# Kernel tuning notes

Measured on AMD Instinct MI355X. Metric: run time of the kernel, lower is better.

The kernel has to match this reference:

```python
import jax, jax.numpy as jnp
import numpy as np

V, E, H, S, B, MAX_OOV = 50000, 256, 512, 500, 64, 50


def setup_inputs() -> dict:
    key = jax.random.key(0)
    ks = jax.random.split(key, 22)
    s = 0.02  # param init scale
    return {
        "input_token": jax.random.randint(ks[0], (B, 1), 0, V),
        "encoder_hidden_states": jax.random.normal(ks[1], (S, B, 2 * H), jnp.float32),
        "projected_encoder_hidden_states": jax.random.normal(ks[2], (S, B, H), jnp.float32),
        "src_mask": jnp.ones((B, S), dtype=bool),
        "prev_hidden": jax.random.normal(ks[3], (1, B, H), jnp.float32),
        "encoder_batch_extended_vocab": jax.random.randint(ks[4], (B, S), 0, V + MAX_OOV),
        "batch_max_oov": MAX_OOV,
        # learned parameters
        "emb": jax.random.normal(ks[5], (V, E), jnp.float32) * s,
        "attn_Wq": jax.random.normal(ks[6], (H, H), jnp.float32) * s,   # query_layer, no bias
        "attn_We": jax.random.normal(ks[7], (1, H), jnp.float32) * s,   # energy_layer, no bias
        "gru_Wih": jax.random.normal(ks[8], (3 * H, E + 2 * H), jnp.float32) * s,
        "gru_Whh": jax.random.normal(ks[9], (3 * H, H), jnp.float32) * s,
        "gru_bih": jax.random.normal(ks[10], (3 * H,), jnp.float32) * s,
        "gru_bhh": jax.random.normal(ks[11], (3 * H,), jnp.float32) * s,
        "lin_W": jax.random.normal(ks[12], (H, E + 3 * H), jnp.float32) * s,
        "lin_b": jax.random.normal(ks[13], (H,), jnp.float32) * s,
        "pg_W": jax.random.normal(ks[14], (1, E + 3 * H), jnp.float32) * s,
        "pg_b": jax.random.normal(ks[15], (1,), jnp.float32) * s,
        "out_W": jax.random.normal(ks[16], (V, H), jnp.float32) * s,
        "out_b": jax.random.normal(ks[17], (V,), jnp.float32) * s,
    }


def _forward(input_token, enc_h, proj_key, prev_hidden, ext_vocab, max_oov,
             emb, attn_Wq, attn_We, gru_Wih, gru_Whh, gru_bih, gru_bhh,
             lin_W, lin_b, pg_W, pg_b, out_W, out_b):
    b = input_token.shape[0]
    embed = jnp.transpose(emb[input_token], (1, 0, 2))  # [1,B,E]

    # Bahdanau attention (softmax over source dim 0; mask unused, as in source)
    q = jnp.einsum('tbh,oh->tbo', prev_hidden, attn_Wq)            # [1,B,H]
    scores = jnp.einsum('sbh,oh->sb', jnp.tanh(q + proj_key), attn_We)  # [S,B]
    alphas = jax.nn.softmax(scores, axis=0)                        # [S,B]
    context = jnp.einsum('sb,sbd->bd', alphas, enc_h)[None]        # [1,B,2H]
    attention_dist = alphas.T                                      # [B,S]

    # GRU cell (torch gate order: r, z, n)
    x = jnp.concatenate([embed, context], axis=2)[0]               # [B,E+2H]
    h = prev_hidden[0]                                             # [B,H]
    gi = x @ gru_Wih.T + gru_bih                                   # [B,3H]
    gh = h @ gru_Whh.T + gru_bhh
    i_r, i_z, i_n = jnp.split(gi, 3, axis=1)
    h_r, h_z, h_n = jnp.split(gh, 3, axis=1)
    r = jax.nn.sigmoid(i_r + h_r)
    z = jax.nn.sigmoid(i_z + h_z)
    n = jnp.tanh(i_n + r * h_n)
    h_new = (1.0 - z) * n + z * h                                  # [B,H]
    rnn_output = h_new[None]                                       # [1,B,H]

    concat = jnp.concatenate([embed, rnn_output, context], axis=2)  # [1,B,E+3H]
    p_gen = jax.nn.sigmoid(jnp.einsum('tbf,of->tbo', concat, pg_W) + pg_b)  # [1,B,1]
    lin = jnp.einsum('tbf,of->tbo', concat, lin_W) + lin_b          # [1,B,H]
    logits = jnp.einsum('tbh,vh->tbv', lin, out_W) + out_b          # [1,B,V]

    gen_prob = p_gen * jax.nn.softmax(logits, axis=2)               # [1,B,V]
    attn_prob = ((1.0 - p_gen) * attention_dist[None])[0]           # [B,S]

    ext = jnp.concatenate(
        [gen_prob, jnp.zeros((1, b, max_oov), gen_prob.dtype)], axis=2) + 1e-12  # [1,B,V+oov]
    rows = jnp.arange(b)[:, None]
    merged = ext.at[0, rows, ext_vocab].add(attn_prob)              # scatter_add over vocab dim
    output = jnp.log(merged)
    return output, h_new[None]


def reference(input_token, encoder_hidden_states, projected_encoder_hidden_states,
              src_mask, prev_hidden, encoder_batch_extended_vocab, batch_max_oov,
              emb, attn_Wq, attn_We, gru_Wih, gru_Whh, gru_bih, gru_bhh,
              lin_W, lin_b, pg_W, pg_b, out_W, out_b):
    return _forward(input_token, encoder_hidden_states, projected_encoder_hidden_states,
                    prev_hidden, encoder_batch_extended_vocab, batch_max_oov,
                    emb, attn_Wq, attn_We, gru_Wih, gru_Whh, gru_bih, gru_bhh,
                    lin_W, lin_b, pg_W, pg_b, out_W, out_b)
```

## Files before the change

kernel.cpp:

```cpp
#include <hip/hip_runtime.h>
#include <hip/hip_bf16.h>
#include <math.h>

namespace {
constexpr int V = 50000, E = 256, H = 512, S = 500, B = 64, OOVN = 50;
constexpr int VEXT = V + OOVN;
constexpr int CCAT = E + 3 * H;
constexpr int G3 = 3 * H;

typedef __attribute__((ext_vector_type(8))) short short8;
typedef __attribute__((ext_vector_type(4))) float f32x4;

__device__ __forceinline__ float wsum(float v) {
#pragma unroll
  for (int off = 32; off > 0; off >>= 1) v += __shfl_xor(v, off, 64);
  return v;
}
__device__ __forceinline__ float sigmoidf(float x) { return 1.f / (1.f + __expf(-x)); }
__device__ __forceinline__ float fast_tanh(float x) {
  x = fminf(fmaxf(x, -15.f), 15.f);
  float e = __expf(2.f * x);
  return __fdividef(e - 1.f, e + 1.f);
}
__device__ __forceinline__ void smerge(float& m, float& l, float om, float ol) {
  float nm = fmaxf(m, om);
  l = l * __expf(m - nm) + ol * __expf(om - nm);
  m = nm;
}

__device__ __forceinline__ short bf16_rn_s(float f) {
  __hip_bfloat16 h = __float2bfloat16(f);
  return __builtin_bit_cast(short, h);
}
__device__ __forceinline__ void hilo1(float f, short* hi, short* lo) {
  unsigned u = __float_as_uint(f);
  *hi = (short)(u >> 16);
  *lo = bf16_rn_s(f - __uint_as_float(u & 0xffff0000u));
}
__device__ __forceinline__ void hilo8(float4 a, float4 b, short8& hi, short8& lo) {
  float f[8] = {a.x, a.y, a.z, a.w, b.x, b.y, b.z, b.w};
#pragma unroll
  for (int i = 0; i < 8; ++i) {
    unsigned u = __float_as_uint(f[i]);
    hi[i] = (short)(u >> 16);
    lo[i] = bf16_rn_s(f[i] - __uint_as_float(u & 0xffff0000u));
  }
}

template <int KSTEPS>
__device__ __forceinline__ void gemm16(const short* __restrict__ Xhi,
                                       const short* __restrict__ Xlo, int ldx, int xk0,
                                       const float* __restrict__ W, int ldw, int wk0,
                                       int n0, const float* __restrict__ bias,
                                       float* __restrict__ C, int ldc) {
  const int l = threadIdx.x & 63;
  const int r16 = l & 15, q16 = l >> 4;
  f32x4 acc[4];
#pragma unroll
  for (int t = 0; t < 4; ++t) acc[t] = (f32x4){0.f, 0.f, 0.f, 0.f};

  const float* wp = W + (size_t)(n0 + r16) * ldw + wk0 + q16 * 8;
  const short* xh[4];
  const short* xl[4];
#pragma unroll
  for (int t = 0; t < 4; ++t) {
    int row = t * 16 + r16;
    xh[t] = Xhi + (size_t)row * ldx + xk0 + q16 * 8;
    xl[t] = Xlo + (size_t)row * ldx + xk0 + q16 * 8;
  }

#pragma unroll
  for (int ks = 0; ks < KSTEPS; ++ks) {
    const int ko = ks * 32;
    float4 w0 = *reinterpret_cast<const float4*>(wp + ko);
    float4 w1 = *reinterpret_cast<const float4*>(wp + ko + 4);
    short8 whi, wlo;
    hilo8(w0, w1, whi, wlo);
#pragma unroll
    for (int t = 0; t < 4; ++t) {
      short8 ah = *reinterpret_cast<const short8*>(xh[t] + ko);
      short8 al = *reinterpret_cast<const short8*>(xl[t] + ko);
      acc[t] = __builtin_amdgcn_mfma_f32_16x16x32_bf16(ah, whi, acc[t], 0, 0, 0);
      acc[t] = __builtin_amdgcn_mfma_f32_16x16x32_bf16(al, whi, acc[t], 0, 0, 0);
      acc[t] = __builtin_amdgcn_mfma_f32_16x16x32_bf16(ah, wlo, acc[t], 0, 0, 0);
    }
  }
  float bv = bias ? bias[n0 + r16] : 0.f;
#pragma unroll
  for (int t = 0; t < 4; ++t) {
#pragma unroll
    for (int r = 0; r < 4; ++r) {
      int row = t * 16 + q16 * 4 + r;
      C[(size_t)row * ldc + n0 + r16] = acc[t][r] + bv;
    }
  }
}

__global__ void k_prep(const int* __restrict__ tok, const float* __restrict__ emb,
                       const float* __restrict__ prevh, float* __restrict__ cc,
                       short* __restrict__ cch, short* __restrict__ ccl,
                       short* __restrict__ hh, short* __restrict__ hl) {
  int i = blockIdx.x * 256 + threadIdx.x;
  hilo1(prevh[i], &hh[i], &hl[i]);
  if (i < 16384) {
    int b = i >> 8, e = i & 255;
    float v = emb[(size_t)tok[b] * E + e];
    cc[b * CCAT + e] = v;
    hilo1(v, &cch[b * CCAT + e], &ccl[b * CCAT + e]);
  }
}

__global__ void __launch_bounds__(256) k_gemm_q(const short* __restrict__ hh,
                                                const short* __restrict__ hl,
                                                const float* __restrict__ Wq,
                                                float* __restrict__ qpart) {
  int w = blockIdx.x * 4 + (threadIdx.x >> 6);
  int c = w >> 5, nt = w & 31;
  gemm16<8>(hh, hl, H, c * 256, Wq, H, c * 256, nt * 16, nullptr,
            qpart + (size_t)c * 64 * H, H);
}

__global__ void k_scores(const float* __restrict__ qpart, const float* __restrict__ pk,
                         const float* __restrict__ We, float* __restrict__ scores) {
  int lane = threadIdx.x & 63;
  int gw = blockIdx.x * 4 + (threadIdx.x >> 6);
  int s = gw >> 6, b = gw & 63;
  const float* q0 = qpart + b * H + lane * 8;
  const float* q1 = q0 + 64 * H;
  const float* kr = pk + ((size_t)s * B + b) * H + lane * 8;
  const float* er = We + lane * 8;
  float part = 0.f;
#pragma unroll
  for (int i = 0; i < 2; ++i) {
    float4 qa = *reinterpret_cast<const float4*>(q0 + i * 4);
    float4 qb = *reinterpret_cast<const float4*>(q1 + i * 4);
    float4 kv = *reinterpret_cast<const float4*>(kr + i * 4);
    float4 ev = *reinterpret_cast<const float4*>(er + i * 4);
    part += fast_tanh(qa.x + qb.x + kv.x) * ev.x + fast_tanh(qa.y + qb.y + kv.y) * ev.y +
            fast_tanh(qa.z + qb.z + kv.z) * ev.z + fast_tanh(qa.w + qb.w + kv.w) * ev.w;
  }
  part = wsum(part);
  if (lane == 0) scores[s * B + b] = part;
}

__global__ void k_softmax_s(const float* __restrict__ scores, float* __restrict__ alphasT) {
  int b = blockIdx.x, t = threadIdx.x;
  int w = t >> 6, lane = t & 63;
  __shared__ float rm[8], rl[8];
  float v = (t < S) ? scores[t * B + b] : -INFINITY;
  float m = v;
#pragma unroll
  for (int off = 32; off > 0; off >>= 1) m = fmaxf(m, __shfl_xor(m, off, 64));
  if (lane == 0) rm[w] = m;
  __syncthreads();
  float bm = rm[0];
#pragma unroll
  for (int i = 1; i < 8; ++i) bm = fmaxf(bm, rm[i]);
  float e = (t < S) ? __expf(v - bm) : 0.f;
  float sw = wsum(e);
  if (lane == 0) rl[w] = sw;
  __syncthreads();
  float tot = rl[0];
#pragma unroll
  for (int i = 1; i < 8; ++i) tot += rl[i];
  if (t < S) alphasT[b * S + t] = e / tot;
}

__global__ void k_ctx(const float* __restrict__ alphasT, const float* __restrict__ ench,
                      float* __restrict__ ctxp) {
  int b = blockIdx.x, chf = blockIdx.y, sh = blockIdx.z;
  int t = threadIdx.x;
  __shared__ float sa[250];
  if (t < 250) sa[t] = alphasT[b * S + sh * 250 + t];
  __syncthreads();
  const float* base = ench + ((size_t)(sh * 250) * B + b) * 1024 + chf * 512 + t;
  float a0 = 0.f, a1 = 0.f;
#pragma unroll 8
  for (int s = 0; s < 250; s += 2) {
    a0 += sa[s] * base[(size_t)s * (B * 1024)];
    a1 += sa[s + 1] * base[(size_t)(s + 1) * (B * 1024)];
  }
  ctxp[((sh * B + b) * 1024) + chf * 512 + t] = a0 + a1;
}

__global__ void k_ctx2(const float* __restrict__ ctxp, float* __restrict__ cc,
                       short* __restrict__ cch, short* __restrict__ ccl) {
  int b = blockIdx.x, t = threadIdx.x;
  int c = t * 4;
  float4 v0 = *reinterpret_cast<const float4*>(&ctxp[(b * 1024) + c]);
  float4 v1 = *reinterpret_cast<const float4*>(&ctxp[((B + b) * 1024) + c]);
  float r[4] = {v0.x + v1.x, v0.y + v1.y, v0.z + v1.z, v0.w + v1.w};
#pragma unroll
  for (int i = 0; i < 4; ++i) {
    int col = 768 + c + i;
    cc[b * CCAT + col] = r[i];
    hilo1(r[i], &cch[b * CCAT + col], &ccl[b * CCAT + col]);
  }
}

__global__ void __launch_bounds__(256) k_gemm_gru(
    const short* __restrict__ cch, const short* __restrict__ ccl,
    const short* __restrict__ hh, const short* __restrict__ hl,
    const float* __restrict__ Wih, const float* __restrict__ Whh,
    float* __restrict__ gip, float* __restrict__ ghp) {
  int w = blockIdx.x * 4 + (threadIdx.x >> 6);
  if (w < 480) {
    int c = w / 96, nt = w % 96;
    int xk0 = (c == 0) ? 0 : 768 + (c - 1) * 256;
    int wk0 = c * 256;
    gemm16<8>(cch, ccl, CCAT, xk0, Wih, 1280, wk0, nt * 16, nullptr,
              gip + (size_t)c * 64 * G3, G3);
  } else {
    int w2 = w - 480;
    int c = w2 / 96, nt = w2 % 96;
    gemm16<8>(hh, hl, H, c * 256, Whh, H, c * 256, nt * 16, nullptr,
              ghp + (size_t)c * 64 * G3, G3);
  }
}

__global__ void k_gates(const float* __restrict__ gip, const float* __restrict__ ghp,
                        const float* __restrict__ bih, const float* __restrict__ bhh,
                        const float* __restrict__ prevh, const float* __restrict__ pgW,
                        const float* __restrict__ pgb, float* __restrict__ cc,
                        short* __restrict__ cch, short* __restrict__ ccl,
                        float* __restrict__ hout, float* __restrict__ pgsum) {
  int b = blockIdx.x, j = threadIdx.x;
  float ir = bih[j], iz = bih[512 + j], in_ = bih[1024 + j];
#pragma unroll
  for (int c = 0; c < 5; ++c) {
    const float* g = gip + (size_t)c * 64 * G3 + b * G3;
    ir += g[j]; iz += g[512 + j]; in_ += g[1024 + j];
  }
  float hr = bhh[j], hz = bhh[512 + j], hn = bhh[1024 + j];
#pragma unroll
  for (int c = 0; c < 2; ++c) {
    const float* g = ghp + (size_t)c * 64 * G3 + b * G3;
    hr += g[j]; hz += g[512 + j]; hn += g[1024 + j];
  }
  float r = sigmoidf(ir + hr);
  float z = sigmoidf(iz + hz);
  float n = fast_tanh(in_ + r * hn);
  float h = prevh[b * H + j];
  float hnew = (1.f - z) * n + z * h;
  hout[b * H + j] = hnew;
  cc[b * CCAT + E + j] = hnew;
  hilo1(hnew, &cch[b * CCAT + E + j], &ccl[b * CCAT + E + j]);
  float acc = hnew * pgW[E + j];
  acc += cc[b * CCAT + 768 + j] * pgW[768 + j];
  acc += cc[b * CCAT + 1280 + j] * pgW[1280 + j];
  if (j < 256) acc += cc[b * CCAT + j] * pgW[j];
  acc = wsum(acc);
  __shared__ float sl[8];
  int w = j >> 6, lane = j & 63;
  if (lane == 0) sl[w] = acc;
  __syncthreads();
  if (j == 0) {
    float tot = pgb[0];
#pragma unroll
    for (int i = 0; i < 8; ++i) tot += sl[i];
    pgsum[b] = tot;
  }
}

__global__ void __launch_bounds__(256) k_gemm_lin(const short* __restrict__ cch,
                                                  const short* __restrict__ ccl,
                                                  const float* __restrict__ linW,
                                                  float* __restrict__ linpart) {
  int w = blockIdx.x * 4 + (threadIdx.x >> 6);
  int c = w >> 5, nt = w & 31;
  gemm16<8>(cch, ccl, CCAT, c * 256, linW, CCAT, c * 256, nt * 16, nullptr,
            linpart + (size_t)c * 64 * H, H);
}

__global__ void k_linfin(const float* __restrict__ linpart, const float* __restrict__ linb,
                         short* __restrict__ lh) {
  int idx = blockIdx.x * 256 + threadIdx.x;
  int b = idx >> 9, o = idx & 511;
  float v = linb[o];
#pragma unroll
  for (int c = 0; c < 7; ++c) v += linpart[(size_t)c * 64 * H + b * H + o];
  lh[idx] = bf16_rn_s(v);
}

__global__ void __launch_bounds__(512, 4) k_gemm_logits(
    const short* __restrict__ lh, const float* __restrict__ outW,
    const float* __restrict__ outb, float* __restrict__ logits) {
  __shared__ __align__(16) short xs[64 * 512];
  char* xb = reinterpret_cast<char*>(xs);
  int tid = threadIdx.x;
#pragma unroll
  for (int k = 0; k < 8; ++k) {
    int m = k * 512 + tid;
    int row = m >> 6;
    short8 v = *reinterpret_cast<const short8*>(lh + (size_t)m * 8);
    int byte = (m * 16) ^ ((row & 7) << 4);
    *reinterpret_cast<short8*>(xb + byte) = v;
  }
  __syncthreads();
  const int l = tid & 63;
  const int r16 = l & 15, q16 = l >> 4;
  const int waveId = blockIdx.x * 8 + (tid >> 6);
  if (waveId >= V / 16) return;
  const int n0 = waveId * 16;
  f32x4 acc[4];
#pragma unroll
  for (int t = 0; t < 4; ++t) acc[t] = (f32x4){0.f, 0.f, 0.f, 0.f};
  const float* wp = outW + (size_t)(n0 + r16) * H + q16 * 8;
  int arow[4], aswz[4];
#pragma unroll
  for (int t = 0; t < 4; ++t) {
    int row = t * 16 + r16;
    arow[t] = row * 1024 + q16 * 16;
    aswz[t] = (row & 7) << 4;
  }
#pragma unroll
  for (int ks = 0; ks < 16; ++ks) {
    float4 w0 = *reinterpret_cast<const float4*>(wp + ks * 32);
    float4 w1 = *reinterpret_cast<const float4*>(wp + ks * 32 + 4);
    short8 wh;
    wh[0] = bf16_rn_s(w0.x); wh[1] = bf16_rn_s(w0.y);
    wh[2] = bf16_rn_s(w0.z); wh[3] = bf16_rn_s(w0.w);
    wh[4] = bf16_rn_s(w1.x); wh[5] = bf16_rn_s(w1.y);
    wh[6] = bf16_rn_s(w1.z); wh[7] = bf16_rn_s(w1.w);
#pragma unroll
    for (int t = 0; t < 4; ++t) {
      short8 a = *reinterpret_cast<const short8*>(xb + ((arow[t] + ks * 64) ^ aswz[t]));
      acc[t] = __builtin_amdgcn_mfma_f32_16x16x32_bf16(a, wh, acc[t], 0, 0, 0);
    }
  }
  float bv = outb[n0 + r16];
#pragma unroll
  for (int t = 0; t < 4; ++t) {
#pragma unroll
    for (int r = 0; r < 4; ++r) {
      int row = t * 16 + q16 * 4 + r;
      logits[(size_t)row * V + n0 + r16] = acc[t][r] + bv;
    }
  }
}

__global__ void k_vmax(const float* __restrict__ logits, float* __restrict__ pm,
                       float* __restrict__ pl) {
  int b = blockIdx.x, c = blockIdx.y, t = threadIdx.x;
  const float* row = logits + (size_t)b * V + c * 5000;
  float m = -INFINITY, l = 0.f;
  for (int i = t; i < 1250; i += 256) {
    float4 v = *reinterpret_cast<const float4*>(&row[i * 4]);
    float mm = fmaxf(fmaxf(v.x, v.y), fmaxf(v.z, v.w));
    float nm = fmaxf(m, mm);
    l = l * __expf(m - nm) + __expf(v.x - nm) + __expf(v.y - nm) + __expf(v.z - nm) +
        __expf(v.w - nm);
    m = nm;
  }
#pragma unroll
  for (int off = 32; off > 0; off >>= 1) {
    float om = __shfl_xor(m, off, 64), ol = __shfl_xor(l, off, 64);
    smerge(m, l, om, ol);
  }
  __shared__ float sm[4], sl[4];
  int w = t >> 6, lane = t & 63;
  if (lane == 0) { sm[w] = m; sl[w] = l; }
  __syncthreads();
  if (t == 0) {
#pragma unroll
    for (int i = 1; i < 4; ++i) smerge(m, l, sm[i], sl[i]);
    pm[b * 10 + c] = m;
    pl[b * 10 + c] = l;
  }
}

__global__ void k_extinit(const float* __restrict__ logits, const float* __restrict__ pm,
                          const float* __restrict__ pl, const float* __restrict__ pgsum,
                          float* __restrict__ out) {
  int b = blockIdx.x, c = blockIdx.y, t = threadIdx.x;
  float m = -INFINITY, l = 0.f;
#pragma unroll
  for (int i = 0; i < 10; ++i) smerge(m, l, pm[b * 10 + i], pl[b * 10 + i]);
  float pg = sigmoidf(pgsum[b]);
  float scale = pg / l;
  const float* lr = logits + (size_t)b * V + c * 5000;
  float* orow = out + (size_t)b * VEXT + c * 5000;
  for (int i = t; i < 2500; i += 256) {
    float2 v = *reinterpret_cast<const float2*>(&lr[i * 2]);
    float2 r;
    r.x = scale * __expf(v.x - m) + 1e-12f;
    r.y = scale * __expf(v.y - m) + 1e-12f;
    *reinterpret_cast<float2*>(&orow[i * 2]) = r;
  }
  if (c == 9 && t < OOVN) out[(size_t)b * VEXT + V + t] = 1e-12f;
}

__constant__ int qbound[5] = {0, 12512, 25024, 37536, 50050};
__global__ void k_scatter_log(const int* __restrict__ extv, const float* __restrict__ alphasT,
                              const float* __restrict__ pgsum, float* __restrict__ out) {
  int b = blockIdx.x >> 2, q = blockIdx.x & 3, t = threadIdx.x;
  int qs0 = qbound[q], qs1 = qbound[q + 1];
  float pg = sigmoidf(pgsum[b]);
  float* row = out + (size_t)b * VEXT;
  for (int s = t; s < S; s += 256) {
    int idx = extv[b * S + s];
    if (idx >= qs0 && idx < qs1) atomicAdd(&row[idx], (1.f - pg) * alphasT[b * S + s]);
  }
  __threadfence();
  __syncthreads();
  int n2 = (qs1 - qs0) >> 1;
  float2* p = reinterpret_cast<float2*>(row + qs0);
  for (int i = t; i < n2; i += 256) {
    float2 v = p[i];
    v.x = logf(v.x);
    v.y = logf(v.y);
    p[i] = v;
  }
  if (((qs1 - qs0) & 1) && t == 0) row[qs1 - 1] = logf(row[qs1 - 1]);
}
}

extern "C" void kernel_launch(void* const* d_in, const int* in_sizes, int n_in,
                              void* d_out, int out_size, void* d_ws, size_t ws_size,
                              hipStream_t stream) {
  const int*   tok   = (const int*)d_in[0];
  const float* ench  = (const float*)d_in[1];
  const float* pk    = (const float*)d_in[2];
  const float* prevh = (const float*)d_in[4];
  const int*   extv  = (const int*)d_in[5];
  const float* emb   = (const float*)d_in[7];
  const float* Wq    = (const float*)d_in[8];
  const float* We    = (const float*)d_in[9];
  const float* Wih   = (const float*)d_in[10];
  const float* Whh   = (const float*)d_in[11];
  const float* bih   = (const float*)d_in[12];
  const float* bhh   = (const float*)d_in[13];
  const float* linW  = (const float*)d_in[14];
  const float* linb  = (const float*)d_in[15];
  const float* pgW   = (const float*)d_in[16];
  const float* pgb   = (const float*)d_in[17];
  const float* outW  = (const float*)d_in[18];
  const float* outb  = (const float*)d_in[19];

  float* out = (float*)d_out;
  float* ws = (float*)d_ws;

  float* qpart   = ws;
  float* scores  = qpart + 65536;
  float* alphasT = scores + 32000;
  float* ctxp    = alphasT + 32000;
  float* cc      = ctxp + 131072;
  float* gip     = cc + 114688;
  float* ghp     = gip + 491520;
  float* linpart = ghp + 196608;
  float* pgsum   = linpart + 229376;
  float* logits  = pgsum + 64;
  float* pm      = logits + 3200000;
  float* pl      = pm + 640;
  short* sp      = (short*)(pl + 640);
  short* cch = sp;
  short* ccl = cch + 114688;
  short* hh  = ccl + 114688;
  short* hl  = hh + 32768;
  short* lh  = hl + 32768;
  float* hout = out + (size_t)B * VEXT;

  k_prep<<<dim3(128), dim3(256), 0, stream>>>(tok, emb, prevh, cc, cch, ccl, hh, hl);
  k_gemm_q<<<dim3(16), dim3(256), 0, stream>>>(hh, hl, Wq, qpart);
  k_scores<<<dim3(8000), dim3(256), 0, stream>>>(qpart, pk, We, scores);
  k_softmax_s<<<dim3(B), dim3(512), 0, stream>>>(scores, alphasT);
  k_ctx<<<dim3(64, 2, 2), dim3(512), 0, stream>>>(alphasT, ench, ctxp);
  k_ctx2<<<dim3(B), dim3(256), 0, stream>>>(ctxp, cc, cch, ccl);
  k_gemm_gru<<<dim3(168), dim3(256), 0, stream>>>(cch, ccl, hh, hl, Wih, Whh, gip, ghp);
  k_gates<<<dim3(B), dim3(512), 0, stream>>>(gip, ghp, bih, bhh, prevh, pgW, pgb, cc, cch,
                                             ccl, hout, pgsum);
  k_gemm_lin<<<dim3(56), dim3(256), 0, stream>>>(cch, ccl, linW, linpart);
  k_linfin<<<dim3(128), dim3(256), 0, stream>>>(linpart, linb, lh);
  k_gemm_logits<<<dim3(391), dim3(512), 0, stream>>>(lh, outW, outb, logits);
  k_vmax<<<dim3(B, 10), dim3(256), 0, stream>>>(logits, pm, pl);
  k_extinit<<<dim3(B, 10), dim3(256), 0, stream>>>(logits, pm, pl, pgsum, out);
  k_scatter_log<<<dim3(256), dim3(256), 0, stream>>>(extv, alphasT, pgsum, out);
}
```

Before: 161.4 us.

## Fuse softmax stats into logits GEMM, merge scatter/log, rebalance GRU/lin GEMMs

The logits GEMM now computes per-block row max and sum-exp partials, which removes the separate vmax pass over the logits. The ext-init, scatter-add and log steps are combined into one kernel that builds each vocab chunk in shared memory, applies the attention scatter there with shared atomics, and writes the log once. This avoids global atomics and the extra read-modify-write passes over the output. The Whh GEMM moves earlier so it runs alongside the query GEMM, now split four ways along K. Most of the lin GEMM moves into the big Wih kernel, leaving only the hidden-state slices after the gates. The trade-off is more launch-time kernels doing mixed work and more partial buffers to reduce.

Result: no change. 162.8 us (+0.8%).

```diff
diff --git a/kernel.cpp b/kernel.cpp
--- a/kernel.cpp
+++ b/kernel.cpp
@@ -7,6 +7,7 @@
 constexpr int VEXT = V + OOVN;
 constexpr int CCAT = E + 3 * H;
 constexpr int G3 = 3 * H;
+constexpr int NLB = 391;
 
 typedef __attribute__((ext_vector_type(8))) short short8;
 typedef __attribute__((ext_vector_type(4))) float f32x4;
@@ -22,8 +23,9 @@
   float e = __expf(2.f * x);
   return __fdividef(e - 1.f, e + 1.f);
 }
-__device__ __forceinline__ void smerge(float& m, float& l, float om, float ol) {
+__device__ __forceinline__ void smerge_s(float& m, float& l, float om, float ol) {
   float nm = fmaxf(m, om);
+  if (nm == -INFINITY) { m = nm; return; }
   l = l * __expf(m - nm) + ol * __expf(om - nm);
   m = nm;
 }
@@ -51,8 +53,7 @@
 __device__ __forceinline__ void gemm16(const short* __restrict__ Xhi,
                                        const short* __restrict__ Xlo, int ldx, int xk0,
                                        const float* __restrict__ W, int ldw, int wk0,
-                                       int n0, const float* __restrict__ bias,
-                                       float* __restrict__ C, int ldc) {
+                                       int n0, float* __restrict__ C, int ldc) {
   const int l = threadIdx.x & 63;
   const int r16 = l & 15, q16 = l >> 4;
   f32x4 acc[4];
@@ -85,13 +86,12 @@
       acc[t] = __builtin_amdgcn_mfma_f32_16x16x32_bf16(ah, wlo, acc[t], 0, 0, 0);
     }
   }
-  float bv = bias ? bias[n0 + r16] : 0.f;
 #pragma unroll
   for (int t = 0; t < 4; ++t) {
 #pragma unroll
     for (int r = 0; r < 4; ++r) {
       int row = t * 16 + q16 * 4 + r;
-      C[(size_t)row * ldc + n0 + r16] = acc[t][r] + bv;
+      C[(size_t)row * ldc + n0 + r16] = acc[t][r];
     }
   }
 }
@@ -110,14 +110,21 @@
   }
 }
 
-__global__ void __launch_bounds__(256) k_gemm_q(const short* __restrict__ hh,
-                                                const short* __restrict__ hl,
-                                                const float* __restrict__ Wq,
-                                                float* __restrict__ qpart) {
+__global__ void __launch_bounds__(256) k_gemm_qgh(
+    const short* __restrict__ hh, const short* __restrict__ hl,
+    const float* __restrict__ Wq, const float* __restrict__ Whh,
+    float* __restrict__ qpart, float* __restrict__ ghp) {
   int w = blockIdx.x * 4 + (threadIdx.x >> 6);
-  int c = w >> 5, nt = w & 31;
-  gemm16<8>(hh, hl, H, c * 256, Wq, H, c * 256, nt * 16, nullptr,
-            qpart + (size_t)c * 64 * H, H);
+  if (w < 128) {
+    int c = w >> 5, nt = w & 31;
+    gemm16<4>(hh, hl, H, c * 128, Wq, H, c * 128, nt * 16,
+              qpart + (size_t)c * 64 * H, H);
+  } else {
+    int w2 = w - 128;
+    int c = w2 / 96, nt = w2 % 96;
+    gemm16<8>(hh, hl, H, c * 256, Whh, H, c * 256, nt * 16,
+              ghp + (size_t)c * 64 * G3, G3);
+  }
 }
 
 __global__ void k_scores(const float* __restrict__ qpart, const float* __restrict__ pk,
@@ -126,18 +133,21 @@
   int gw = blockIdx.x * 4 + (threadIdx.x >> 6);
   int s = gw >> 6, b = gw & 63;
   const float* q0 = qpart + b * H + lane * 8;
-  const float* q1 = q0 + 64 * H;
   const float* kr = pk + ((size_t)s * B + b) * H + lane * 8;
   const float* er = We + lane * 8;
   float part = 0.f;
 #pragma unroll
   for (int i = 0; i < 2; ++i) {
     float4 qa = *reinterpret_cast<const float4*>(q0 + i * 4);
-    float4 qb = *reinterpret_cast<const float4*>(q1 + i * 4);
+    float4 qb = *reinterpret_cast<const float4*>(q0 + 64 * H + i * 4);
+    float4 qc = *reinterpret_cast<const float4*>(q0 + 128 * H + i * 4);
+    float4 qd = *reinterpret_cast<const float4*>(q0 + 192 * H + i * 4);
     float4 kv = *reinterpret_cast<const float4*>(kr + i * 4);
     float4 ev = *reinterpret_cast<const float4*>(er + i * 4);
-    part += fast_tanh(qa.x + qb.x + kv.x) * ev.x + fast_tanh(qa.y + qb.y + kv.y) * ev.y +
-            fast_tanh(qa.z + qb.z + kv.z) * ev.z + fast_tanh(qa.w + qb.w + kv.w) * ev.w;
+    part += fast_tanh(qa.x + qb.x + qc.x + qd.x + kv.x) * ev.x +
+            fast_tanh(qa.y + qb.y + qc.y + qd.y + kv.y) * ev.y +
+            fast_tanh(qa.z + qb.z + qc.z + qd.z + kv.z) * ev.z +
+            fast_tanh(qa.w + qb.w + qc.w + qd.w + kv.w) * ev.w;
   }
   part = wsum(part);
   if (lane == 0) scores[s * B + b] = part;
@@ -198,23 +208,23 @@
   }
 }
 
-__global__ void __launch_bounds__(256) k_gemm_gru(
+__global__ void __launch_bounds__(256) k_gemm_big(
     const short* __restrict__ cch, const short* __restrict__ ccl,
-    const short* __restrict__ hh, const short* __restrict__ hl,
-    const float* __restrict__ Wih, const float* __restrict__ Whh,
-    float* __restrict__ gip, float* __restrict__ ghp) {
+    const float* __restrict__ Wih, const float* __restrict__ linW,
+    float* __restrict__ gip, float* __restrict__ linpart) {
   int w = blockIdx.x * 4 + (threadIdx.x >> 6);
   if (w < 480) {
     int c = w / 96, nt = w % 96;
     int xk0 = (c == 0) ? 0 : 768 + (c - 1) * 256;
     int wk0 = c * 256;
-    gemm16<8>(cch, ccl, CCAT, xk0, Wih, 1280, wk0, nt * 16, nullptr,
+    gemm16<8>(cch, ccl, CCAT, xk0, Wih, 1280, wk0, nt * 16,
               gip + (size_t)c * 64 * G3, G3);
   } else {
     int w2 = w - 480;
-    int c = w2 / 96, nt = w2 % 96;
-    gemm16<8>(hh, hl, H, c * 256, Whh, H, c * 256, nt * 16, nullptr,
-              ghp + (size_t)c * 64 * G3, G3);
+    int c = w2 >> 5, nt = w2 & 31;
+    int k0 = (c == 0) ? 0 : 768 + (c - 1) * 256;
+    gemm16<8>(cch, ccl, CCAT, k0, linW, CCAT, k0, nt * 16,
+              linpart + (size_t)c * 64 * H, H);
   }
 }
 
@@ -262,14 +272,15 @@
   }
 }
 
-__global__ void __launch_bounds__(256) k_gemm_lin(const short* __restrict__ cch,
-                                                  const short* __restrict__ ccl,
-                                                  const float* __restrict__ linW,
-                                                  float* __restrict__ linpart) {
+__global__ void __launch_bounds__(256) k_gemm_linh(const short* __restrict__ cch,
+                                                   const short* __restrict__ ccl,
+                                                   const float* __restrict__ linW,
+                                                   float* __restrict__ linpart) {
   int w = blockIdx.x * 4 + (threadIdx.x >> 6);
   int c = w >> 5, nt = w & 31;
-  gemm16<8>(cch, ccl, CCAT, c * 256, linW, CCAT, c * 256, nt * 16, nullptr,
-            linpart + (size_t)c * 64 * H, H);
+  int k0 = 256 + c * 256;
+  gemm16<8>(cch, ccl, CCAT, k0, linW, CCAT, k0, nt * 16,
+            linpart + (size_t)(5 + c) * 64 * H, H);
 }
 
 __global__ void k_linfin(const float* __restrict__ linpart, const float* __restrict__ linb,
@@ -282,10 +293,12 @@
   lh[idx] = bf16_rn_s(v);
 }
 
-__global__ void __launch_bounds__(512, 4) k_gemm_logits(
+__global__ void __launch_bounds__(512) k_gemm_logits(
     const short* __restrict__ lh, const float* __restrict__ outW,
-    const float* __restrict__ outb, float* __restrict__ logits) {
+    const float* __restrict__ outb, float* __restrict__ logits,
+    float* __restrict__ pm, float* __restrict__ pl) {
   __shared__ __align__(16) short xs[64 * 512];
+  __shared__ float pml[8][64][2];
   char* xb = reinterpret_cast<char*>(xs);
   int tid = threadIdx.x;
 #pragma unroll
@@ -299,119 +312,110 @@
   __syncthreads();
   const int l = tid & 63;
   const int r16 = l & 15, q16 = l >> 4;
-  const int waveId = blockIdx.x * 8 + (tid >> 6);
-  if (waveId >= V / 16) return;
-  const int n0 = waveId * 16;
-  f32x4 acc[4];
-#pragma unroll
-  for (int t = 0; t < 4; ++t) acc[t] = (f32x4){0.f, 0.f, 0.f, 0.f};
-  const float* wp = outW + (size_t)(n0 + r16) * H + q16 * 8;
-  int arow[4], aswz[4];
-#pragma unroll
-  for (int t = 0; t < 4; ++t) {
-    int row = t * 16 + r16;
-    arow[t] = row * 1024 + q16 * 16;
-    aswz[t] = (row & 7) << 4;
-  }
-#pragma unroll
-  for (int ks = 0; ks < 16; ++ks) {
-    float4 w0 = *reinterpret_cast<const float4*>(wp + ks * 32);
-    float4 w1 = *reinterpret_cast<const float4*>(wp + ks * 32 + 4);
-    short8 wh;
-    wh[0] = bf16_rn_s(w0.x); wh[1] = bf16_rn_s(w0.y);
-    wh[2] = bf16_rn_s(w0.z); wh[3] = bf16_rn_s(w0.w);
-    wh[4] = bf16_rn_s(w1.x); wh[5] = bf16_rn_s(w1.y);
-    wh[6] = bf16_rn_s(w1.z); wh[7] = bf16_rn_s(w1.w);
+  const int wid = tid >> 6;
+  const int waveId = blockIdx.x * 8 + wid;
+  const bool active = waveId < V / 16;
+  if (active) {
+    const int n0 = waveId * 16;
+    f32x4 acc[4];
+#pragma unroll
+    for (int t = 0; t < 4; ++t) acc[t] = (f32x4){0.f, 0.f, 0.f, 0.f};
+    const float* wp = outW + (size_t)(n0 + r16) * H + q16 * 8;
+    int arow[4], aswz[4];
 #pragma unroll
     for (int t = 0; t < 4; ++t) {
-      short8 a = *reinterpret_cast<const short8*>(xb + ((arow[t] + ks * 64) ^ aswz[t]));
-      acc[t] = __builtin_amdgcn_mfma_f32_16x16x32_bf16(a, wh, acc[t], 0, 0, 0);
+      int row = t * 16 + r16;
+      arow[t] = row * 1024 + q16 * 16;
+      aswz[t] = (row & 7) << 4;
     }
-  }
-  float bv = outb[n0 + r16];
-#pragma unroll
-  for (int t = 0; t < 4; ++t) {
-#pragma unroll
-    for (int r = 0; r < 4; ++r) {
-      int row = t * 16 + q16 * 4 + r;
-      logits[(size_t)row * V + n0 + r16] = acc[t][r] + bv;
+#pragma unroll
+    for (int ks = 0; ks < 16; ++ks) {
+      float4 w0 = *reinterpret_cast<const float4*>(wp + ks * 32);
+      float4 w1 = *reinterpret_cast<const float4*>(wp + ks * 32 + 4);
+      short8 wh;
+      wh[0] = bf16_rn_s(w0.x); wh[1] = bf16_rn_s(w0.y);
+      wh[2] = bf16_rn_s(w0.z); wh[3] = bf16_rn_s(w0.w);
+      wh[4] = bf16_rn_s(w1.x); wh[5] = bf16_rn_s(w1.y);
+      wh[6] = bf16_rn_s(w1.z); wh[7] = bf16_rn_s(w1.w);
+#pragma unroll
+      for (int t = 0; t < 4; ++t) {
+        short8 a = *reinterpret_cast<const short8*>(xb + ((arow[t] + ks * 64) ^ aswz[t]));
+        acc[t] = __builtin_amdgcn_mfma_f32_16x16x32_bf16(a, wh, acc[t], 0, 0, 0);
+      }
     }
-  }
-}
-
-__global__ void k_vmax(const float* __restrict__ logits, float* __restrict__ pm,
-                       float* __restrict__ pl) {
+    float bv = outb[n0 + r16];
+#pragma unroll
+    for (int t = 0; t < 4; ++t) {
+#pragma unroll
+      for (int r = 0; r < 4; ++r) {
+        float y = acc[t][r] + bv;
+        int row = t * 16 + q16 * 4 + r;
+        logits[(size_t)row * V + n0 + r16] = y;
+        float m = y;
+#pragma unroll
+        for (int off = 8; off > 0; off >>= 1) m = fmaxf(m, __shfl_xor(m, off, 64));
+        float e = __expf(y - m);
+#pragma unroll
+        for (int off = 8; off > 0; off >>= 1) e += __shfl_xor(e, off, 64);
+        if (r16 == 0) { pml[wid][row][0] = m; pml[wid][row][1] = e; }
+      }
+    }
+  } else if (r16 == 0) {
+#pragma unroll
+    for (int t = 0; t < 4; ++t)
+#pragma unroll
+      for (int r = 0; r < 4; ++r) {
+        int row = t * 16 + q16 * 4 + r;
+        pml[wid][row][0] = -INFINITY;
+        pml[wid][row][1] = 0.f;
+      }
+  }
+  __syncthreads();
+  if (tid < 64) {
+    float m = pml[0][tid][0], lv = pml[0][tid][1];
+#pragma unroll
+    for (int i = 1; i < 8; ++i) smerge_s(m, lv, pml[i][tid][0], pml[i][tid][1]);
+    pm[blockIdx.x * 64 + tid] = m;
+    pl[blockIdx.x * 64 + tid] = lv;
+  }
+}
+
+__global__ void k_final(const float* __restrict__ logits, const float* __restrict__ pm,
+                        const float* __restrict__ pl, const float* __restrict__ pgsum,
+                        const int* __restrict__ extv, const float* __restrict__ alphasT,
+                        float* __restrict__ out) {
   int b = blockIdx.x, c = blockIdx.y, t = threadIdx.x;
-  const float* row = logits + (size_t)b * V + c * 5000;
-  float m = -INFINITY, l = 0.f;
-  for (int i = t; i < 1250; i += 256) {
-    float4 v = *reinterpret_cast<const float4*>(&row[i * 4]);
-    float mm = fmaxf(fmaxf(v.x, v.y), fmaxf(v.z, v.w));
-    float nm = fmaxf(m, mm);
-    l = l * __expf(m - nm) + __expf(v.x - nm) + __expf(v.y - nm) + __expf(v.z - nm) +
-        __expf(v.w - nm);
-    m = nm;
-  }
+  __shared__ float sp_[5056];
+  __shared__ float rm[4], rl[4];
+  float m = -INFINITY, lv = 0.f;
+  for (int i = t; i < NLB; i += 256) smerge_s(m, lv, pm[i * 64 + b], pl[i * 64 + b]);
 #pragma unroll
   for (int off = 32; off > 0; off >>= 1) {
-    float om = __shfl_xor(m, off, 64), ol = __shfl_xor(l, off, 64);
-    smerge(m, l, om, ol);
-  }
-  __shared__ float sm[4], sl[4];
+    float om = __shfl_xor(m, off, 64), ol = __shfl_xor(lv, off, 64);
+    smerge_s(m, lv, om, ol);
+  }
   int w = t >> 6, lane = t & 63;
-  if (lane == 0) { sm[w] = m; sl[w] = l; }
-  __syncthreads();
-  if (t == 0) {
-#pragma unroll
-    for (int i = 1; i < 4; ++i) smerge(m, l, sm[i], sl[i]);
-    pm[b * 10 + c] = m;
-    pl[b * 10 + c] = l;
-  }
-}
-
-__global__ void k_extinit(const float* __restrict__ logits, const float* __restrict__ pm,
-                          const float* __restrict__ pl, const float* __restrict__ pgsum,
-                          float* __restrict__ out) {
-  int b = blockIdx.x, c = blockIdx.y, t = threadIdx.x;
-  float m = -INFINITY, l = 0.f;
-#pragma unroll
-  for (int i = 0; i < 10; ++i) smerge(m, l, pm[b * 10 + i], pl[b * 10 + i]);
+  if (lane == 0) { rm[w] = m; rl[w] = lv; }
+  __syncthreads();
+  m = rm[0]; lv = rl[0];
+#pragma unroll
+  for (int i = 1; i < 4; ++i) smerge_s(m, lv, rm[i], rl[i]);
   float pg = sigmoidf(pgsum[b]);
-  float scale = pg / l;
-  const float* lr = logits + (size_t)b * V + c * 5000;
-  float* orow = out + (size_t)b * VEXT + c * 5000;
-  for (int i = t; i < 2500; i += 256) {
-    float2 v = *reinterpret_cast<const float2*>(&lr[i * 2]);
-    float2 r;
-    r.x = scale * __expf(v.x - m) + 1e-12f;
-    r.y = scale * __expf(v.y - m) + 1e-12f;
-    *reinterpret_cast<float2*>(&orow[i * 2]) = r;
-  }
-  if (c == 9 && t < OOVN) out[(size_t)b * VEXT + V + t] = 1e-12f;
-}
-
-__constant__ int qbound[5] = {0, 12512, 25024, 37536, 50050};
-__global__ void k_scatter_log(const int* __restrict__ extv, const float* __restrict__ alphasT,
-                              const float* __restrict__ pgsum, float* __restrict__ out) {
-  int b = blockIdx.x >> 2, q = blockIdx.x & 3, t = threadIdx.x;
-  int qs0 = qbound[q], qs1 = qbound[q + 1];
-  float pg = sigmoidf(pgsum[b]);
-  float* row = out + (size_t)b * VEXT;
+  float scale = pg / lv;
+  const int base = c * 5000;
+  const int len = (c == 9) ? 5050 : 5000;
+  const float* lr = logits + (size_t)b * V + base;
+  for (int i = t; i < len; i += 256)
+    sp_[i] = (i < 5000) ? scale * __expf(lr[i] - m) + 1e-12f : 1e-12f;
+  __syncthreads();
+  float wgt = 1.f - pg;
   for (int s = t; s < S; s += 256) {
-    int idx = extv[b * S + s];
-    if (idx >= qs0 && idx < qs1) atomicAdd(&row[idx], (1.f - pg) * alphasT[b * S + s]);
-  }
-  __threadfence();
-  __syncthreads();
-  int n2 = (qs1 - qs0) >> 1;
-  float2* p = reinterpret_cast<float2*>(row + qs0);
-  for (int i = t; i < n2; i += 256) {
-    float2 v = p[i];
-    v.x = logf(v.x);
-    v.y = logf(v.y);
-    p[i] = v;
-  }
-  if (((qs1 - qs0) & 1) && t == 0) row[qs1 - 1] = logf(row[qs1 - 1]);
+    int idx = extv[b * S + s] - base;
+    if ((unsigned)idx < (unsigned)len) atomicAdd(&sp_[idx], wgt * alphasT[b * S + s]);
+  }
+  __syncthreads();
+  float* orow = out + (size_t)b * VEXT + base;
+  for (int i = t; i < len; i += 256) orow[i] = logf(sp_[i]);
 }
 }
 
@@ -441,7 +445,7 @@
   float* ws = (float*)d_ws;
 
   float* qpart   = ws;
-  float* scores  = qpart + 65536;
+  float* scores  = qpart + 131072;
   float* alphasT = scores + 32000;
   float* ctxp    = alphasT + 32000;
   float* cc      = ctxp + 131072;
@@ -451,8 +455,8 @@
   float* pgsum   = linpart + 229376;
   float* logits  = pgsum + 64;
   float* pm      = logits + 3200000;
-  float* pl      = pm + 640;
-  short* sp      = (short*)(pl + 640);
+  float* pl      = pm + 25024;
+  short* sp      = (short*)(pl + 25024);
   short* cch = sp;
   short* ccl = cch + 114688;
   short* hh  = ccl + 114688;
@@ -461,18 +465,16 @@
   float* hout = out + (size_t)B * VEXT;
 
   k_prep<<<dim3(128), dim3(256), 0, stream>>>(tok, emb, prevh, cc, cch, ccl, hh, hl);
-  k_gemm_q<<<dim3(16), dim3(256), 0, stream>>>(hh, hl, Wq, qpart);
+  k_gemm_qgh<<<dim3(80), dim3(256), 0, stream>>>(hh, hl, Wq, Whh, qpart, ghp);
   k_scores<<<dim3(8000), dim3(256), 0, stream>>>(qpart, pk, We, scores);
   k_softmax_s<<<dim3(B), dim3(512), 0, stream>>>(scores, alphasT);
   k_ctx<<<dim3(64, 2, 2), dim3(512), 0, stream>>>(alphasT, ench, ctxp);
   k_ctx2<<<dim3(B), dim3(256), 0, stream>>>(ctxp, cc, cch, ccl);
-  k_gemm_gru<<<dim3(168), dim3(256), 0, stream>>>(cch, ccl, hh, hl, Wih, Whh, gip, ghp);
+  k_gemm_big<<<dim3(160), dim3(256), 0, stream>>>(cch, ccl, Wih, linW, gip, linpart);
   k_gates<<<dim3(B), dim3(512), 0, stream>>>(gip, ghp, bih, bhh, prevh, pgW, pgb, cc, cch,
                                              ccl, hout, pgsum);
-  k_gemm_lin<<<dim3(56), dim3(256), 0, stream>>>(cch, ccl, linW, linpart);
+  k_gemm_linh<<<dim3(16), dim3(256), 0, stream>>>(cch, ccl, linW, linpart);
   k_linfin<<<dim3(128), dim3(256), 0, stream>>>(linpart, linb, lh);
-  k_gemm_logits<<<dim3(391), dim3(512), 0, stream>>>(lh, outW, outb, logits);
-  k_vmax<<<dim3(B, 10), dim3(256), 0, stream>>>(logits, pm, pl);
-  k_extinit<<<dim3(B, 10), dim3(256), 0, stream>>>(logits, pm, pl, pgsum, out);
-  k_scatter_log<<<dim3(256), dim3(256), 0, stream>>>(extv, alphasT, pgsum, out);
-}
+  k_gemm_logits<<<dim3(NLB), dim3(512), 0, stream>>>(lh, outW, outb, logits, pm, pl);
+  k_final<<<dim3(B, 10), dim3(256), 0, stream>>>(logits, pm, pl, pgsum, extv, alphasT, out);
+}
```
